# Optimization experiments

Measured on AMD Instinct MI355X. Metric: run time of the kernel, lower is better.

The kernel has to match this reference:

```python
import jax, jax.numpy as jnp
import numpy as np

HIDDEN = 1024
HEADS = 16
HEAD_DIM = HIDDEN // HEADS


def setup_inputs() -> dict:
    key = jax.random.key(0)
    kx, kq, kk, kv, ko = jax.random.split(key, 5)
    s = 1.0 / np.sqrt(HIDDEN)
    return {
        "x": jax.random.normal(kx, (2, 2048, HIDDEN), dtype=jnp.float32),
        "Wq": jax.random.normal(kq, (HIDDEN, HIDDEN), dtype=jnp.float32) * s,
        "Wk": jax.random.normal(kk, (HIDDEN, HIDDEN), dtype=jnp.float32) * s,
        "Wv": jax.random.normal(kv, (HIDDEN, HIDDEN), dtype=jnp.float32) * s,
        "Wo": jax.random.normal(ko, (HIDDEN, HIDDEN), dtype=jnp.float32) * s,
    }


def reference(x, Wq, Wk, Wv, Wo):
    B, T, C = x.shape
    H, D = HEADS, HEAD_DIM
    # projections (torch Linear: y = x @ W.T); weights here stored as (out,in)==(C,C)
    q = (x @ Wq.T).reshape(B, T, H, D)
    k = (x @ Wk.T).reshape(B, T, H, D)
    v = (x @ Wv.T).reshape(B, T, H, D)
    scale = 1.0 / np.sqrt(D).astype(np.float32)
    # scores: (B,H,T,T)
    attn = jnp.einsum("bqhd,bkhd->bhqk", q, k) * scale
    causal = jnp.tril(jnp.ones((T, T), dtype=bool))  # keep lower triangle
    attn = jnp.where(causal, attn, -jnp.inf)
    attn = jax.nn.softmax(attn, axis=-1)
    out = jnp.einsum("bhqk,bkhd->bqhd", attn, v).reshape(B, T, C)
    return out @ Wo.T
```

## Files before the change

### kernel.cpp

```cpp
#include <hip/hip_runtime.h>
#include <cstdint>
#include <cstddef>

#define HID 1024
#define NH 16
#define HD 64
#define SEQ 2048
#define BATCH 2

typedef __attribute__((ext_vector_type(8))) short bf16x8;
typedef __attribute__((ext_vector_type(4))) short bf16x4;
typedef bf16x8 __attribute__((may_alias)) bf16x8_ma;
typedef bf16x4 __attribute__((may_alias)) bf16x4_ma;
typedef uint4 __attribute__((may_alias)) uint4_ma;
typedef __attribute__((ext_vector_type(4))) float f32x4;

__device__ __forceinline__ unsigned short f2bf(float f){
  unsigned u = __builtin_bit_cast(unsigned, f);
  u += 0x7fffu + ((u >> 16) & 1u);
  return (unsigned short)(u >> 16);
}

__device__ __forceinline__ unsigned cvtpk_bf16(float lo, float hi){
  unsigned r;
  asm("v_cvt_pk_bf16_f32 %0, %1, %2" : "=v"(r) : "v"(lo), "v"(hi));
  return r;
}

__device__ __forceinline__ void gll(const unsigned short* g, unsigned short* l){
  __builtin_amdgcn_global_load_lds(
      (const __attribute__((address_space(1))) unsigned int*)(g),
      (__attribute__((address_space(3))) unsigned int*)(l),
      16, 0, 0);
}

__global__ __launch_bounds__(256) void cvt_all(
    const float* __restrict__ x,  const float* __restrict__ wq,
    const float* __restrict__ wk, const float* __restrict__ wv,
    const float* __restrict__ wo,
    unsigned short* __restrict__ xb,  unsigned short* __restrict__ wqb,
    unsigned short* __restrict__ wkb, unsigned short* __restrict__ wvb,
    unsigned short* __restrict__ wob)
{
  const size_t NX = (size_t)BATCH*SEQ*HID;
  const size_t NW = (size_t)HID*HID;
  size_t i = ((size_t)blockIdx.x*256 + threadIdx.x)*4;
  const float* src; unsigned short* dst; size_t off;
  if (i < NX) { src = x; dst = xb; off = i; }
  else {
    size_t j = i - NX; int w = (int)(j >> 20); off = j & (NW-1);
    if      (w==0){ src=wq; dst=wqb; }
    else if (w==1){ src=wk; dst=wkb; }
    else if (w==2){ src=wv; dst=wvb; }
    else          { src=wo; dst=wob; }
  }
  float4 v = *(const float4*)(src+off);
  uint2 p;
  p.x = (unsigned)f2bf(v.x) | ((unsigned)f2bf(v.y)<<16);
  p.y = (unsigned)f2bf(v.z) | ((unsigned)f2bf(v.w)<<16);
  *(uint2*)(dst+off) = p;
}

__global__ __launch_bounds__(256) void gemm_qkv(
    const unsigned short* __restrict__ A,
    const unsigned short* __restrict__ Bq,
    const unsigned short* __restrict__ Bk,
    const unsigned short* __restrict__ Bv,
    unsigned short* __restrict__ Qh,
    unsigned short* __restrict__ Kh,
    unsigned short* __restrict__ VhT)
{
  __shared__ unsigned short S[16384];
  const int tid = threadIdx.x;
  const int w = tid >> 6, lane = tid & 63, l15 = lane & 15, quad = lane >> 4;
  const int wm = (w >> 1)*64, wn = (w & 1)*64;
  const int bm = blockIdx.y*128;
  const int which = blockIdx.x >> 3;
  const int bn = (blockIdx.x & 7)*128;
  const unsigned short* B = which==0 ? Bq : (which==1 ? Bk : Bv);
  unsigned short* C       = which==0 ? Qh : (which==1 ? Kh : VhT);
  const float cscale      = which==0 ? 0.18033688011112042f : 1.0f;
  const int lrow = lane >> 2, lcol = (lane & 3)*8;

  f32x4 acc[4][4] = {};

  {
    #pragma unroll
    for (int p=0;p<2;p++){
      int c = w*2 + p;
      gll(&A[(size_t)(bm + c*16 + lrow)*HID + lcol], &S[c*512]);
      gll(&B[(size_t)(bn + c*16 + lrow)*HID + lcol], &S[8192 + c*512]);
    }
  }
  __syncthreads();

  int cur = 0;
  for (int kb=0; kb<32; ++kb){
    if (kb < 31){
      unsigned short* Ad = S + (cur^1)*4096;
      unsigned short* Bd = S + 8192 + (cur^1)*4096;
      #pragma unroll
      for (int p=0;p<2;p++){
        int c = w*2 + p;
        gll(&A[(size_t)(bm + c*16 + lrow)*HID + (kb+1)*32 + lcol], &Ad[c*512]);
        gll(&B[(size_t)(bn + c*16 + lrow)*HID + (kb+1)*32 + lcol], &Bd[c*512]);
      }
    }
    const unsigned short* Ac = S + cur*4096;
    const unsigned short* Bc = S + 8192 + cur*4096;
    bf16x8 af[4], bfr[4];
    #pragma unroll
    for (int i=0;i<4;i++) af[i]  = *(const bf16x8*)(&Ac[(wm + i*16 + l15)*32 + quad*8]);
    #pragma unroll
    for (int j=0;j<4;j++) bfr[j] = *(const bf16x8*)(&Bc[(wn + j*16 + l15)*32 + quad*8]);
    #pragma unroll
    for (int i=0;i<4;i++)
      #pragma unroll
      for (int j=0;j<4;j++)
        acc[i][j] = __builtin_amdgcn_mfma_f32_16x16x32_bf16(af[i], bfr[j], acc[i][j], 0,0,0);
    __syncthreads();
    cur ^= 1;
  }

  #pragma unroll
  for (int i=0;i<4;i++)
    #pragma unroll
    for (int j=0;j<4;j++)
      #pragma unroll
      for (int r=0;r<4;r++){
        int row = wm + i*16 + quad*4 + r;
        int col = wn + j*16 + l15;
        unsigned off = (unsigned)(row*256 + col*2);
        *(unsigned short*)((char*)S + (off ^ ((unsigned)(row & 7) << 4))) =
            f2bf(acc[i][j][r]*cscale);
      }
  __syncthreads();
  if (which < 2){
    #pragma unroll
    for (int pass=0; pass<8; ++pass){
      int tr    = pass*16 + (tid >> 4);
      int hf    = (tid >> 3) & 1;
      int blkin = tid & 7;
      unsigned off = (unsigned)(tr*256 + hf*128 + blkin*16);
      uint4 v = *(const uint4_ma*)((const char*)S + (off ^ ((unsigned)(tr & 7) << 4)));
      int m = bm + tr, b = m >> 11, t = m & (SEQ-1);
      int h = (bn >> 6) + hf;
      *(uint4*)(&C[(((size_t)(b*NH + h))*SEQ + t)*HD + blkin*8]) = v;
    }
  } else {
    const int b = bm >> 11, tb = bm & (SEQ-1);
    #pragma unroll
    for (int pass=0; pass<8; ++pass){
      int idx  = pass*256 + tid;
      int dcol = idx & 127;
      int tc   = idx >> 7;
      unsigned short tmp[8];
      #pragma unroll
      for (int j=0;j<8;j++){
        int r = tc*8 + j;
        unsigned off = (unsigned)(r*256 + dcol*2) ^ ((unsigned)j << 4);
        tmp[j] = *(const unsigned short*)((const char*)S + off);
      }
      int hh = (bn >> 6) + (dcol >> 6);
      int d  = dcol & 63;
      *(uint4*)(&C[(((size_t)(b*NH + hh))*HD + d)*SEQ + tb + tc*8]) = *(uint4_ma*)tmp;
    }
  }
}

__global__ __launch_bounds__(256) void gemm_out(
    const unsigned short* __restrict__ A,
    const unsigned short* __restrict__ B,
    float* __restrict__ C)
{
  __shared__ unsigned short As[8192];
  __shared__ unsigned short Bs[4096];
  const int tid = threadIdx.x;
  const int w = tid >> 6, lane = tid & 63, l15 = lane & 15, quad = lane >> 4;
  const int wm = (w >> 1)*64, wn = (w & 1)*32;
  const int bm = blockIdx.y*128, bn = blockIdx.x*64;
  const int lrow = lane >> 2, lcol = (lane & 3)*8;

  f32x4 acc[4][2] = {};
  for (int kb=0; kb<16; ++kb){
    __syncthreads();
    #pragma unroll
    for (int p=0;p<4;p++){
      int c = p*4 + w;
      int h = c >> 3, rb = c & 7;
      gll(&A[(size_t)(bm + rb*16 + lrow)*HID + kb*64 + h*32 + lcol], &As[h*4096 + rb*512]);
    }
    #pragma unroll
    for (int p=0;p<2;p++){
      int c = p*4 + w;
      int h = c >> 2, rb = c & 3;
      gll(&B[(size_t)(bn + rb*16 + lrow)*HID + kb*64 + h*32 + lcol], &Bs[h*2048 + rb*512]);
    }
    __syncthreads();
    #pragma unroll
    for (int kc=0;kc<2;kc++){
      bf16x8 af[4], bfr[2];
      #pragma unroll
      for (int i=0;i<4;i++) af[i]  = *(const bf16x8*)(&As[kc*4096 + (wm + i*16 + l15)*32 + quad*8]);
      #pragma unroll
      for (int j=0;j<2;j++) bfr[j] = *(const bf16x8*)(&Bs[kc*2048 + (wn + j*16 + l15)*32 + quad*8]);
      #pragma unroll
      for (int i=0;i<4;i++)
        #pragma unroll
        for (int j=0;j<2;j++)
          acc[i][j] = __builtin_amdgcn_mfma_f32_16x16x32_bf16(af[i], bfr[j], acc[i][j], 0,0,0);
    }
  }
  #pragma unroll
  for (int i=0;i<4;i++)
    #pragma unroll
    for (int j=0;j<2;j++)
      #pragma unroll
      for (int r=0;r<4;r++){
        int m = bm + wm + i*16 + quad*4 + r;
        int n = bn + wn + j*16 + l15;
        C[(size_t)m*HID + n] = acc[i][j][r];
      }
}

__global__ __launch_bounds__(256, 4) void attn(
    const unsigned short* __restrict__ Qh,
    const unsigned short* __restrict__ Kh,
    const unsigned short* __restrict__ VhT,
    unsigned short* __restrict__ Ao)
{
  __shared__ unsigned short QP[4096];
  __shared__ unsigned short Ks[2][4096];
  __shared__ unsigned short Vt[2][4096];

  const int bh = blockIdx.x;
  const int y  = blockIdx.y;
  const int tid = threadIdx.x;
  const int w = tid >> 6, lane = tid & 63, l15 = lane & 15, quad = lane >> 4;
  const int lrow = lane >> 2, lcol = (lane & 3)*8;

  const size_t base = (size_t)bh * SEQ * HD;
  const unsigned short* VTg = VhT + base;
  unsigned short* Psw = QP + w*1024;
  const unsigned swz = (unsigned)(l15 & 7) << 4;
  const int b = bh >> 4, h = bh & (NH-1);

  #pragma unroll 1
  for (int hf=0; hf<2; ++hf){
    const int qb = hf ? (31 - y) : y;
    const unsigned short* Qg = Qh + base + (size_t)qb*64*HD;

    __syncthreads();

    #pragma unroll
    for (int p=0;p<2;p++){
      int c = w*2 + p;
      gll(&Qg[(size_t)((c&3)*16 + lrow)*HD + (c>>2)*32 + lcol], &QP[(c>>2)*2048 + (c&3)*512]);
    }
    {
      const unsigned short* Kg = Kh + base;
      if (w < 2){
        #pragma unroll
        for (int p=0;p<4;p++){ int cc = w*4 + p;
          gll(&Kg[(size_t)((cc&3)*16 + lrow)*HD + (cc>>2)*32 + lcol], &Ks[0][(cc>>2)*2048 + (cc&3)*512]); }
      } else {
        #pragma unroll
        for (int p=0;p<4;p++){ int cc = (w-2)*4 + p;
          gll(&VTg[(size_t)((cc&3)*16 + lrow)*SEQ + (cc>>2)*32 + lcol], &Vt[0][(cc>>2)*2048 + (cc&3)*512]); }
      }
    }
    __syncthreads();
    bf16x8 qfrag[2];
    #pragma unroll
    for (int kc=0;kc<2;kc++)
      qfrag[kc] = *(const bf16x8*)(&QP[kc*2048 + (w*16 + l15)*32 + quad*8]);
    __syncthreads();

    f32x4 lacc = {0.f, 0.f, 0.f, 0.f};
    f32x4 oacc[4] = {};
    const int qrow = qb*64 + w*16 + l15;
    int cur = 0;

    for (int kb=0; kb<=qb; ++kb){
      if (kb < qb){
        const unsigned short* Kg2 = Kh + base + (size_t)(kb+1)*64*HD;
        unsigned short* Kd = Ks[cur^1];
        unsigned short* Vd = Vt[cur^1];
        if (w < 2){
          #pragma unroll
          for (int p=0;p<4;p++){ int cc = w*4 + p;
            gll(&Kg2[(size_t)((cc&3)*16 + lrow)*HD + (cc>>2)*32 + lcol], &Kd[(cc>>2)*2048 + (cc&3)*512]); }
        } else {
          #pragma unroll
          for (int p=0;p<4;p++){ int cc = (w-2)*4 + p;
            gll(&VTg[(size_t)((cc&3)*16 + lrow)*SEQ + (size_t)(kb+1)*64 + (cc>>2)*32 + lcol], &Vd[(cc>>2)*2048 + (cc&3)*512]); }
        }
      }

      const unsigned short* Ksc = Ks[cur];
      f32x4 s[4] = {};
      #pragma unroll
      for (int cb=0;cb<4;cb++)
        #pragma unroll
        for (int kc=0;kc<2;kc++){
          bf16x8 kfr = *(const bf16x8*)(&Ksc[kc*2048 + (cb*16 + l15)*32 + quad*8]);
          s[cb] = __builtin_amdgcn_mfma_f32_16x16x32_bf16(kfr, qfrag[kc], s[cb], 0,0,0);
        }

      if (kb == qb){
        #pragma unroll
        for (int cb=0;cb<4;cb++)
          #pragma unroll
          for (int r=0;r<4;r++){
            int t = kb*64 + cb*16 + quad*4 + r;
            if (t > qrow) s[cb][r] = -1e30f;
          }
      }
      #pragma unroll
      for (int cb=0;cb<4;cb++)
        #pragma unroll
        for (int r=0;r<4;r++)
          s[cb][r] = exp2f(s[cb][r]);
      lacc += (s[0] + s[1]) + (s[2] + s[3]);

      #pragma unroll
      for (int cb=0;cb<4;cb++){
        uint2 d2;
        d2.x = cvtpk_bf16(s[cb][0], s[cb][1]);
        d2.y = cvtpk_bf16(s[cb][2], s[cb][3]);
        *(bf16x4_ma*)((char*)Psw + (((unsigned)(l15*128 + cb*32 + quad*8)) ^ swz)) =
            __builtin_bit_cast(bf16x4, d2);
      }
      asm volatile("" ::: "memory");
      bf16x8 pa[2];
      #pragma unroll
      for (int kc=0;kc<2;kc++)
        pa[kc] = *(const bf16x8_ma*)((const char*)Psw + (((unsigned)(l15*128 + kc*64 + quad*16)) ^ swz));

      const unsigned short* Vtc = Vt[cur];
      #pragma unroll
      for (int db=0;db<4;db++)
        #pragma unroll
        for (int kc=0;kc<2;kc++){
          bf16x8 vfr = *(const bf16x8*)(&Vtc[kc*2048 + (db*16 + l15)*32 + quad*8]);
          oacc[db] = __builtin_amdgcn_mfma_f32_16x16x32_bf16(pa[kc], vfr, oacc[db], 0,0,0);
        }

      if (kb < qb) __syncthreads();
      cur ^= 1;
    }

    float l = (lacc[0] + lacc[1]) + (lacc[2] + lacc[3]);
    l += __shfl_xor(l, 16);
    l += __shfl_xor(l, 32);
    float inv[4];
    #pragma unroll
    for (int r=0;r<4;r++)
      inv[r] = 1.0f / __shfl(l, quad*4 + r);

    #pragma unroll
    for (int db=0;db<4;db++)
      #pragma unroll
      for (int r=0;r<4;r++){
        int t = qb*64 + w*16 + quad*4 + r;
        int col = h*HD + db*16 + l15;
        Ao[((size_t)b*SEQ + t)*HID + col] = f2bf(oacc[db][r] * inv[r]);
      }
  }
}

extern "C" void kernel_launch(void* const* d_in, const int* in_sizes, int n_in,
                              void* d_out, int out_size, void* d_ws, size_t ws_size,
                              hipStream_t stream)
{
  const float* x  = (const float*)d_in[0];
  const float* Wq = (const float*)d_in[1];
  const float* Wk = (const float*)d_in[2];
  const float* Wv = (const float*)d_in[3];
  const float* Wo = (const float*)d_in[4];

  unsigned short* xb  = (unsigned short*)d_ws;
  unsigned short* wqb = xb  + (size_t)4*1024*1024;
  unsigned short* wkb = wqb + (size_t)1024*1024;
  unsigned short* wvb = wkb + (size_t)1024*1024;
  unsigned short* wob = wvb + (size_t)1024*1024;
  unsigned short* Qh  = wob + (size_t)1024*1024;
  unsigned short* Kh  = Qh  + (size_t)4*1024*1024;
  unsigned short* Vh  = Kh  + (size_t)4*1024*1024;
  unsigned short* VhT = Vh  + (size_t)4*1024*1024;
  unsigned short* Ao  = xb;

  cvt_all<<<8192, 256, 0, stream>>>(x, Wq, Wk, Wv, Wo, xb, wqb, wkb, wvb, wob);

  gemm_qkv<<<dim3(24, 32), 256, 0, stream>>>(xb, wqb, wkb, wvb, Qh, Kh, VhT);

  attn<<<dim3(BATCH*NH, 16), 256, 0, stream>>>(Qh, Kh, VhT, Ao);

  gemm_out<<<dim3(16, 32), 256, 0, stream>>>(Ao, wob, (float*)d_out);
}
```

Baseline: 178.7 us.

## Triple-buffer K/V in attention, one query block per workgroup with balanced ordering

```diff
diff --git a/kernel.cpp b/kernel.cpp
--- a/kernel.cpp
+++ b/kernel.cpp
@@ -223,150 +223,156 @@
       }
 }
 
-__global__ __launch_bounds__(256, 4) void attn(
+__global__ __launch_bounds__(256, 2) void attn(
     const unsigned short* __restrict__ Qh,
     const unsigned short* __restrict__ Kh,
     const unsigned short* __restrict__ VhT,
     unsigned short* __restrict__ Ao)
 {
   __shared__ unsigned short QP[4096];
-  __shared__ unsigned short Ks[2][4096];
-  __shared__ unsigned short Vt[2][4096];
+  __shared__ unsigned short Ks[3][4096];
+  __shared__ unsigned short Vt[3][4096];
 
   const int bh = blockIdx.x;
   const int y  = blockIdx.y;
+  const int a = y & 7, bb = y >> 3;
+  const int qb = (bb & 1) ? (7 - a)*4 + bb : a*4 + bb;
   const int tid = threadIdx.x;
   const int w = tid >> 6, lane = tid & 63, l15 = lane & 15, quad = lane >> 4;
   const int lrow = lane >> 2, lcol = (lane & 3)*8;
 
   const size_t base = (size_t)bh * SEQ * HD;
+  const unsigned short* Qg  = Qh + base + (size_t)qb*64*HD;
+  const unsigned short* Kg  = Kh + base;
   const unsigned short* VTg = VhT + base;
   unsigned short* Psw = QP + w*1024;
   const unsigned swz = (unsigned)(l15 & 7) << 4;
-  const int b = bh >> 4, h = bh & (NH-1);
-
-  #pragma unroll 1
-  for (int hf=0; hf<2; ++hf){
-    const int qb = hf ? (31 - y) : y;
-    const unsigned short* Qg = Qh + base + (size_t)qb*64*HD;
-
-    __syncthreads();
-
-    #pragma unroll
-    for (int p=0;p<2;p++){
-      int c = w*2 + p;
-      gll(&Qg[(size_t)((c&3)*16 + lrow)*HD + (c>>2)*32 + lcol], &QP[(c>>2)*2048 + (c&3)*512]);
-    }
+
+  #pragma unroll
+  for (int p=0;p<2;p++){
+    int c = w*2 + p;
+    gll(&Qg[(size_t)((c&3)*16 + lrow)*HD + (c>>2)*32 + lcol], &QP[(c>>2)*2048 + (c&3)*512]);
+  }
+  {
+    const int t1 = qb > 0 ? 1 : 0;
+    if (w < 2){
+      #pragma unroll
+      for (int p=0;p<4;p++){ int cc = w*4 + p;
+        gll(&Kg[(size_t)((cc&3)*16 + lrow)*HD + (cc>>2)*32 + lcol], &Ks[0][(cc>>2)*2048 + (cc&3)*512]); }
+      #pragma unroll
+      for (int p=0;p<4;p++){ int cc = w*4 + p;
+        gll(&Kg[(size_t)(t1*64 + (cc&3)*16 + lrow)*HD + (cc>>2)*32 + lcol], &Ks[1][(cc>>2)*2048 + (cc&3)*512]); }
+    } else {
+      #pragma unroll
+      for (int p=0;p<4;p++){ int cc = (w-2)*4 + p;
+        gll(&VTg[(size_t)((cc&3)*16 + lrow)*SEQ + (cc>>2)*32 + lcol], &Vt[0][(cc>>2)*2048 + (cc&3)*512]); }
+      #pragma unroll
+      for (int p=0;p<4;p++){ int cc = (w-2)*4 + p;
+        gll(&VTg[(size_t)((cc&3)*16 + lrow)*SEQ + t1*64 + (cc>>2)*32 + lcol], &Vt[1][(cc>>2)*2048 + (cc&3)*512]); }
+    }
+  }
+  __syncthreads();
+  bf16x8 qfrag[2];
+  #pragma unroll
+  for (int kc=0;kc<2;kc++)
+    qfrag[kc] = *(const bf16x8*)(&QP[kc*2048 + (w*16 + l15)*32 + quad*8]);
+  __syncthreads();
+
+  f32x4 lacc = {0.f, 0.f, 0.f, 0.f};
+  f32x4 oacc[4] = {};
+  const int qrow = qb*64 + w*16 + l15;
+
+  unsigned short *K0 = Ks[0], *K1 = Ks[1], *K2 = Ks[2];
+  unsigned short *V0 = Vt[0], *V1 = Vt[1], *V2 = Vt[2];
+
+  for (int kb=0; kb<=qb; ++kb){
     {
-      const unsigned short* Kg = Kh + base;
+      const int tn = (kb+2 <= qb) ? (kb+2) : qb;
       if (w < 2){
         #pragma unroll
         for (int p=0;p<4;p++){ int cc = w*4 + p;
-          gll(&Kg[(size_t)((cc&3)*16 + lrow)*HD + (cc>>2)*32 + lcol], &Ks[0][(cc>>2)*2048 + (cc&3)*512]); }
+          gll(&Kg[(size_t)(tn*64 + (cc&3)*16 + lrow)*HD + (cc>>2)*32 + lcol], &K2[(cc>>2)*2048 + (cc&3)*512]); }
       } else {
         #pragma unroll
         for (int p=0;p<4;p++){ int cc = (w-2)*4 + p;
-          gll(&VTg[(size_t)((cc&3)*16 + lrow)*SEQ + (cc>>2)*32 + lcol], &Vt[0][(cc>>2)*2048 + (cc&3)*512]); }
-      }
-    }
-    __syncthreads();
-    bf16x8 qfrag[2];
-    #pragma unroll
-    for (int kc=0;kc<2;kc++)
-      qfrag[kc] = *(const bf16x8*)(&QP[kc*2048 + (w*16 + l15)*32 + quad*8]);
-    __syncthreads();
-
-    f32x4 lacc = {0.f, 0.f, 0.f, 0.f};
-    f32x4 oacc[4] = {};
-    const int qrow = qb*64 + w*16 + l15;
-    int cur = 0;
-
-    for (int kb=0; kb<=qb; ++kb){
-      if (kb < qb){
-        const unsigned short* Kg2 = Kh + base + (size_t)(kb+1)*64*HD;
-        unsigned short* Kd = Ks[cur^1];
-        unsigned short* Vd = Vt[cur^1];
-        if (w < 2){
-          #pragma unroll
-          for (int p=0;p<4;p++){ int cc = w*4 + p;
-            gll(&Kg2[(size_t)((cc&3)*16 + lrow)*HD + (cc>>2)*32 + lcol], &Kd[(cc>>2)*2048 + (cc&3)*512]); }
-        } else {
-          #pragma unroll
-          for (int p=0;p<4;p++){ int cc = (w-2)*4 + p;
-            gll(&VTg[(size_t)((cc&3)*16 + lrow)*SEQ + (size_t)(kb+1)*64 + (cc>>2)*32 + lcol], &Vd[(cc>>2)*2048 + (cc&3)*512]); }
-        }
-      }
-
-      const unsigned short* Ksc = Ks[cur];
-      f32x4 s[4] = {};
+          gll(&VTg[(size_t)((cc&3)*16 + lrow)*SEQ + (size_t)tn*64 + (cc>>2)*32 + lcol], &V2[(cc>>2)*2048 + (cc&3)*512]); }
+      }
+    }
+    __builtin_amdgcn_sched_barrier(0);
+
+    f32x4 s[4] = {};
+    #pragma unroll
+    for (int cb=0;cb<4;cb++)
+      #pragma unroll
+      for (int kc=0;kc<2;kc++){
+        bf16x8 kfr = *(const bf16x8*)(&K0[kc*2048 + (cb*16 + l15)*32 + quad*8]);
+        s[cb] = __builtin_amdgcn_mfma_f32_16x16x32_bf16(kfr, qfrag[kc], s[cb], 0,0,0);
+      }
+
+    if (kb == qb){
       #pragma unroll
       for (int cb=0;cb<4;cb++)
         #pragma unroll
-        for (int kc=0;kc<2;kc++){
-          bf16x8 kfr = *(const bf16x8*)(&Ksc[kc*2048 + (cb*16 + l15)*32 + quad*8]);
-          s[cb] = __builtin_amdgcn_mfma_f32_16x16x32_bf16(kfr, qfrag[kc], s[cb], 0,0,0);
+        for (int r=0;r<4;r++){
+          int t = kb*64 + cb*16 + quad*4 + r;
+          if (t > qrow) s[cb][r] = -1e30f;
         }
-
-      if (kb == qb){
-        #pragma unroll
-        for (int cb=0;cb<4;cb++)
-          #pragma unroll
-          for (int r=0;r<4;r++){
-            int t = kb*64 + cb*16 + quad*4 + r;
-            if (t > qrow) s[cb][r] = -1e30f;
-          }
-      }
-      #pragma unroll
-      for (int cb=0;cb<4;cb++)
-        #pragma unroll
-        for (int r=0;r<4;r++)
-          s[cb][r] = exp2f(s[cb][r]);
-      lacc += (s[0] + s[1]) + (s[2] + s[3]);
-
-      #pragma unroll
-      for (int cb=0;cb<4;cb++){
-        uint2 d2;
-        d2.x = cvtpk_bf16(s[cb][0], s[cb][1]);
-        d2.y = cvtpk_bf16(s[cb][2], s[cb][3]);
-        *(bf16x4_ma*)((char*)Psw + (((unsigned)(l15*128 + cb*32 + quad*8)) ^ swz)) =
-            __builtin_bit_cast(bf16x4, d2);
-      }
-      asm volatile("" ::: "memory");
-      bf16x8 pa[2];
-      #pragma unroll
-      for (int kc=0;kc<2;kc++)
-        pa[kc] = *(const bf16x8_ma*)((const char*)Psw + (((unsigned)(l15*128 + kc*64 + quad*16)) ^ swz));
-
-      const unsigned short* Vtc = Vt[cur];
-      #pragma unroll
-      for (int db=0;db<4;db++)
-        #pragma unroll
-        for (int kc=0;kc<2;kc++){
-          bf16x8 vfr = *(const bf16x8*)(&Vtc[kc*2048 + (db*16 + l15)*32 + quad*8]);
-          oacc[db] = __builtin_amdgcn_mfma_f32_16x16x32_bf16(pa[kc], vfr, oacc[db], 0,0,0);
-        }
-
-      if (kb < qb) __syncthreads();
-      cur ^= 1;
-    }
-
-    float l = (lacc[0] + lacc[1]) + (lacc[2] + lacc[3]);
-    l += __shfl_xor(l, 16);
-    l += __shfl_xor(l, 32);
-    float inv[4];
-    #pragma unroll
-    for (int r=0;r<4;r++)
-      inv[r] = 1.0f / __shfl(l, quad*4 + r);
+    }
+    #pragma unroll
+    for (int cb=0;cb<4;cb++)
+      #pragma unroll
+      for (int r=0;r<4;r++)
+        s[cb][r] = exp2f(s[cb][r]);
+    lacc += (s[0] + s[1]) + (s[2] + s[3]);
+
+    #pragma unroll
+    for (int cb=0;cb<4;cb++){
+      uint2 d2;
+      d2.x = cvtpk_bf16(s[cb][0], s[cb][1]);
+      d2.y = cvtpk_bf16(s[cb][2], s[cb][3]);
+      *(bf16x4_ma*)((char*)Psw + (((unsigned)(l15*128 + cb*32 + quad*8)) ^ swz)) =
+          __builtin_bit_cast(bf16x4, d2);
+    }
+    asm volatile("" ::: "memory");
+    bf16x8 pa[2];
+    #pragma unroll
+    for (int kc=0;kc<2;kc++)
+      pa[kc] = *(const bf16x8_ma*)((const char*)Psw + (((unsigned)(l15*128 + kc*64 + quad*16)) ^ swz));
 
     #pragma unroll
     for (int db=0;db<4;db++)
       #pragma unroll
-      for (int r=0;r<4;r++){
-        int t = qb*64 + w*16 + quad*4 + r;
-        int col = h*HD + db*16 + l15;
-        Ao[((size_t)b*SEQ + t)*HID + col] = f2bf(oacc[db][r] * inv[r]);
-      }
-  }
+      for (int kc=0;kc<2;kc++){
+        bf16x8 vfr = *(const bf16x8*)(&V0[kc*2048 + (db*16 + l15)*32 + quad*8]);
+        oacc[db] = __builtin_amdgcn_mfma_f32_16x16x32_bf16(pa[kc], vfr, oacc[db], 0,0,0);
+      }
+
+    asm volatile("s_waitcnt vmcnt(4)" ::: "memory");
+    __builtin_amdgcn_s_barrier();
+    __builtin_amdgcn_sched_barrier(0);
+
+    unsigned short* tk = K0; K0 = K1; K1 = K2; K2 = tk;
+    unsigned short* tv = V0; V0 = V1; V1 = V2; V2 = tv;
+  }
+  asm volatile("s_waitcnt vmcnt(0)" ::: "memory");
+
+  float l = (lacc[0] + lacc[1]) + (lacc[2] + lacc[3]);
+  l += __shfl_xor(l, 16);
+  l += __shfl_xor(l, 32);
+  float inv[4];
+  #pragma unroll
+  for (int r=0;r<4;r++)
+    inv[r] = 1.0f / __shfl(l, quad*4 + r);
+
+  const int b = bh >> 4, h = bh & (NH-1);
+  #pragma unroll
+  for (int db=0;db<4;db++)
+    #pragma unroll
+    for (int r=0;r<4;r++){
+      int t = qb*64 + w*16 + quad*4 + r;
+      int col = h*HD + db*16 + l15;
+      Ao[((size_t)b*SEQ + t)*HID + col] = f2bf(oacc[db][r] * inv[r]);
+    }
 }
 
 extern "C" void kernel_launch(void* const* d_in, const int* in_sizes, int n_in,
@@ -394,7 +400,7 @@
 
   gemm_qkv<<<dim3(24, 32), 256, 0, stream>>>(xb, wqb, wkb, wvb, Qh, Kh, VhT);
 
-  attn<<<dim3(BATCH*NH, 16), 256, 0, stream>>>(Qh, Kh, VhT, Ao);
+  attn<<<dim3(BATCH*NH, SEQ/64), 256, 0, stream>>>(Qh, Kh, VhT, Ao);
 
   gemm_out<<<dim3(16, 32), 256, 0, stream>>>(Ao, wob, (float*)d_out);
 }
```

New measurement: 185.7 us. 1.04x slower.

## Double-buffer output GEMM loads and split attention into one query block per workgroup

Applied to the files above, without the earlier changes.

```diff
diff --git a/kernel.cpp b/kernel.cpp
--- a/kernel.cpp
+++ b/kernel.cpp
@@ -173,8 +173,7 @@
     const unsigned short* __restrict__ B,
     float* __restrict__ C)
 {
-  __shared__ unsigned short As[8192];
-  __shared__ unsigned short Bs[4096];
+  __shared__ unsigned short S[12288];
   const int tid = threadIdx.x;
   const int w = tid >> 6, lane = tid & 63, l15 = lane & 15, quad = lane >> 4;
   const int wm = (w >> 1)*64, wn = (w & 1)*32;
@@ -182,35 +181,45 @@
   const int lrow = lane >> 2, lcol = (lane & 3)*8;
 
   f32x4 acc[4][2] = {};
-  for (int kb=0; kb<16; ++kb){
+
+  {
+    #pragma unroll
+    for (int p=0;p<2;p++){
+      int c = w*2 + p;
+      gll(&A[(size_t)(bm + c*16 + lrow)*HID + lcol], &S[c*512]);
+    }
+    gll(&B[(size_t)(bn + w*16 + lrow)*HID + lcol], &S[8192 + w*512]);
+  }
+  __syncthreads();
+
+  int cur = 0;
+  for (int kb=0; kb<32; ++kb){
+    if (kb < 31){
+      unsigned short* Ad = S + (cur^1)*4096;
+      unsigned short* Bd = S + 8192 + (cur^1)*2048;
+      #pragma unroll
+      for (int p=0;p<2;p++){
+        int c = w*2 + p;
+        gll(&A[(size_t)(bm + c*16 + lrow)*HID + (kb+1)*32 + lcol], &Ad[c*512]);
+      }
+      gll(&B[(size_t)(bn + w*16 + lrow)*HID + (kb+1)*32 + lcol], &Bd[w*512]);
+    }
+    const unsigned short* Ac = S + cur*4096;
+    const unsigned short* Bc = S + 8192 + cur*2048;
+    bf16x8 af[4], bfr[2];
+    #pragma unroll
+    for (int i=0;i<4;i++) af[i]  = *(const bf16x8*)(&Ac[(wm + i*16 + l15)*32 + quad*8]);
+    #pragma unroll
+    for (int j=0;j<2;j++) bfr[j] = *(const bf16x8*)(&Bc[(wn + j*16 + l15)*32 + quad*8]);
+    #pragma unroll
+    for (int i=0;i<4;i++)
+      #pragma unroll
+      for (int j=0;j<2;j++)
+        acc[i][j] = __builtin_amdgcn_mfma_f32_16x16x32_bf16(af[i], bfr[j], acc[i][j], 0,0,0);
     __syncthreads();
-    #pragma unroll
-    for (int p=0;p<4;p++){
-      int c = p*4 + w;
-      int h = c >> 3, rb = c & 7;
-      gll(&A[(size_t)(bm + rb*16 + lrow)*HID + kb*64 + h*32 + lcol], &As[h*4096 + rb*512]);
-    }
-    #pragma unroll
-    for (int p=0;p<2;p++){
-      int c = p*4 + w;
-      int h = c >> 2, rb = c & 3;
-      gll(&B[(size_t)(bn + rb*16 + lrow)*HID + kb*64 + h*32 + lcol], &Bs[h*2048 + rb*512]);
-    }
-    __syncthreads();
-    #pragma unroll
-    for (int kc=0;kc<2;kc++){
-      bf16x8 af[4], bfr[2];
-      #pragma unroll
-      for (int i=0;i<4;i++) af[i]  = *(const bf16x8*)(&As[kc*4096 + (wm + i*16 + l15)*32 + quad*8]);
-      #pragma unroll
-      for (int j=0;j<2;j++) bfr[j] = *(const bf16x8*)(&Bs[kc*2048 + (wn + j*16 + l15)*32 + quad*8]);
-      #pragma unroll
-      for (int i=0;i<4;i++)
-        #pragma unroll
-        for (int j=0;j<2;j++)
-          acc[i][j] = __builtin_amdgcn_mfma_f32_16x16x32_bf16(af[i], bfr[j], acc[i][j], 0,0,0);
-    }
-  }
+    cur ^= 1;
+  }
+
   #pragma unroll
   for (int i=0;i<4;i++)
     #pragma unroll
@@ -235,138 +244,133 @@
 
   const int bh = blockIdx.x;
   const int y  = blockIdx.y;
+  const int a = y & 7, bb = y >> 3;
+  const int qb = (bb & 1) ? (7 - a)*4 + bb : a*4 + bb;
   const int tid = threadIdx.x;
   const int w = tid >> 6, lane = tid & 63, l15 = lane & 15, quad = lane >> 4;
   const int lrow = lane >> 2, lcol = (lane & 3)*8;
 
   const size_t base = (size_t)bh * SEQ * HD;
+  const unsigned short* Qg  = Qh + base + (size_t)qb*64*HD;
   const unsigned short* VTg = VhT + base;
   unsigned short* Psw = QP + w*1024;
   const unsigned swz = (unsigned)(l15 & 7) << 4;
-  const int b = bh >> 4, h = bh & (NH-1);
-
-  #pragma unroll 1
-  for (int hf=0; hf<2; ++hf){
-    const int qb = hf ? (31 - y) : y;
-    const unsigned short* Qg = Qh + base + (size_t)qb*64*HD;
-
-    __syncthreads();
-
-    #pragma unroll
-    for (int p=0;p<2;p++){
-      int c = w*2 + p;
-      gll(&Qg[(size_t)((c&3)*16 + lrow)*HD + (c>>2)*32 + lcol], &QP[(c>>2)*2048 + (c&3)*512]);
-    }
-    {
-      const unsigned short* Kg = Kh + base;
+
+  #pragma unroll
+  for (int p=0;p<2;p++){
+    int c = w*2 + p;
+    gll(&Qg[(size_t)((c&3)*16 + lrow)*HD + (c>>2)*32 + lcol], &QP[(c>>2)*2048 + (c&3)*512]);
+  }
+  {
+    const unsigned short* Kg = Kh + base;
+    if (w < 2){
+      #pragma unroll
+      for (int p=0;p<4;p++){ int cc = w*4 + p;
+        gll(&Kg[(size_t)((cc&3)*16 + lrow)*HD + (cc>>2)*32 + lcol], &Ks[0][(cc>>2)*2048 + (cc&3)*512]); }
+    } else {
+      #pragma unroll
+      for (int p=0;p<4;p++){ int cc = (w-2)*4 + p;
+        gll(&VTg[(size_t)((cc&3)*16 + lrow)*SEQ + (cc>>2)*32 + lcol], &Vt[0][(cc>>2)*2048 + (cc&3)*512]); }
+    }
+  }
+  __syncthreads();
+  bf16x8 qfrag[2];
+  #pragma unroll
+  for (int kc=0;kc<2;kc++)
+    qfrag[kc] = *(const bf16x8*)(&QP[kc*2048 + (w*16 + l15)*32 + quad*8]);
+  __syncthreads();
+
+  f32x4 lacc = {0.f, 0.f, 0.f, 0.f};
+  f32x4 oacc[4] = {};
+  const int qrow = qb*64 + w*16 + l15;
+  int cur = 0;
+
+  for (int kb=0; kb<=qb; ++kb){
+    if (kb < qb){
+      const unsigned short* Kg2 = Kh + base + (size_t)(kb+1)*64*HD;
+      unsigned short* Kd = Ks[cur^1];
+      unsigned short* Vd = Vt[cur^1];
       if (w < 2){
         #pragma unroll
         for (int p=0;p<4;p++){ int cc = w*4 + p;
-          gll(&Kg[(size_t)((cc&3)*16 + lrow)*HD + (cc>>2)*32 + lcol], &Ks[0][(cc>>2)*2048 + (cc&3)*512]); }
+          gll(&Kg2[(size_t)((cc&3)*16 + lrow)*HD + (cc>>2)*32 + lcol], &Kd[(cc>>2)*2048 + (cc&3)*512]); }
       } else {
         #pragma unroll
         for (int p=0;p<4;p++){ int cc = (w-2)*4 + p;
-          gll(&VTg[(size_t)((cc&3)*16 + lrow)*SEQ + (cc>>2)*32 + lcol], &Vt[0][(cc>>2)*2048 + (cc&3)*512]); }
-      }
-    }
-    __syncthreads();
-    bf16x8 qfrag[2];
-    #pragma unroll
-    for (int kc=0;kc<2;kc++)
-      qfrag[kc] = *(const bf16x8*)(&QP[kc*2048 + (w*16 + l15)*32 + quad*8]);
-    __syncthreads();
-
-    f32x4 lacc = {0.f, 0.f, 0.f, 0.f};
-    f32x4 oacc[4] = {};
-    const int qrow = qb*64 + w*16 + l15;
-    int cur = 0;
-
-    for (int kb=0; kb<=qb; ++kb){
-      if (kb < qb){
-        const unsigned short* Kg2 = Kh + base + (size_t)(kb+1)*64*HD;
-        unsigned short* Kd = Ks[cur^1];
-        unsigned short* Vd = Vt[cur^1];
-        if (w < 2){
-          #pragma unroll
-          for (int p=0;p<4;p++){ int cc = w*4 + p;
-            gll(&Kg2[(size_t)((cc&3)*16 + lrow)*HD + (cc>>2)*32 + lcol], &Kd[(cc>>2)*2048 + (cc&3)*512]); }
-        } else {
-          #pragma unroll
-          for (int p=0;p<4;p++){ int cc = (w-2)*4 + p;
-            gll(&VTg[(size_t)((cc&3)*16 + lrow)*SEQ + (size_t)(kb+1)*64 + (cc>>2)*32 + lcol], &Vd[(cc>>2)*2048 + (cc&3)*512]); }
-        }
-      }
-
-      const unsigned short* Ksc = Ks[cur];
-      f32x4 s[4] = {};
+          gll(&VTg[(size_t)((cc&3)*16 + lrow)*SEQ + (size_t)(kb+1)*64 + (cc>>2)*32 + lcol], &Vd[(cc>>2)*2048 + (cc&3)*512]); }
+      }
+    }
+
+    const unsigned short* Ksc = Ks[cur];
+    f32x4 s[4] = {};
+    #pragma unroll
+    for (int cb=0;cb<4;cb++)
+      #pragma unroll
+      for (int kc=0;kc<2;kc++){
+        bf16x8 kfr = *(const bf16x8*)(&Ksc[kc*2048 + (cb*16 + l15)*32 + quad*8]);
+        s[cb] = __builtin_amdgcn_mfma_f32_16x16x32_bf16(kfr, qfrag[kc], s[cb], 0,0,0);
+      }
+
+    if (kb == qb){
       #pragma unroll
       for (int cb=0;cb<4;cb++)
         #pragma unroll
-        for (int kc=0;kc<2;kc++){
-          bf16x8 kfr = *(const bf16x8*)(&Ksc[kc*2048 + (cb*16 + l15)*32 + quad*8]);
-          s[cb] = __builtin_amdgcn_mfma_f32_16x16x32_bf16(kfr, qfrag[kc], s[cb], 0,0,0);
+        for (int r=0;r<4;r++){
+          int t = kb*64 + cb*16 + quad*4 + r;
+          if (t > qrow) s[cb][r] = -1e30f;
         }
-
-      if (kb == qb){
-        #pragma unroll
-        for (int cb=0;cb<4;cb++)
-          #pragma unroll
-          for (int r=0;r<4;r++){
-            int t = kb*64 + cb*16 + quad*4 + r;
-            if (t > qrow) s[cb][r] = -1e30f;
-          }
-      }
-      #pragma unroll
-      for (int cb=0;cb<4;cb++)
-        #pragma unroll
-        for (int r=0;r<4;r++)
-          s[cb][r] = exp2f(s[cb][r]);
-      lacc += (s[0] + s[1]) + (s[2] + s[3]);
-
-      #pragma unroll
-      for (int cb=0;cb<4;cb++){
-        uint2 d2;
-        d2.x = cvtpk_bf16(s[cb][0], s[cb][1]);
-        d2.y = cvtpk_bf16(s[cb][2], s[cb][3]);
-        *(bf16x4_ma*)((char*)Psw + (((unsigned)(l15*128 + cb*32 + quad*8)) ^ swz)) =
-            __builtin_bit_cast(bf16x4, d2);
-      }
-      asm volatile("" ::: "memory");
-      bf16x8 pa[2];
-      #pragma unroll
-      for (int kc=0;kc<2;kc++)
-        pa[kc] = *(const bf16x8_ma*)((const char*)Psw + (((unsigned)(l15*128 + kc*64 + quad*16)) ^ swz));
-
-      const unsigned short* Vtc = Vt[cur];
-      #pragma unroll
-      for (int db=0;db<4;db++)
-        #pragma unroll
-        for (int kc=0;kc<2;kc++){
-          bf16x8 vfr = *(const bf16x8*)(&Vtc[kc*2048 + (db*16 + l15)*32 + quad*8]);
-          oacc[db] = __builtin_amdgcn_mfma_f32_16x16x32_bf16(pa[kc], vfr, oacc[db], 0,0,0);
-        }
-
-      if (kb < qb) __syncthreads();
-      cur ^= 1;
-    }
-
-    float l = (lacc[0] + lacc[1]) + (lacc[2] + lacc[3]);
-    l += __shfl_xor(l, 16);
-    l += __shfl_xor(l, 32);
-    float inv[4];
-    #pragma unroll
-    for (int r=0;r<4;r++)
-      inv[r] = 1.0f / __shfl(l, quad*4 + r);
-
+    }
+    #pragma unroll
+    for (int cb=0;cb<4;cb++)
+      #pragma unroll
+      for (int r=0;r<4;r++)
+        s[cb][r] = exp2f(s[cb][r]);
+    lacc += (s[0] + s[1]) + (s[2] + s[3]);
+
+    #pragma unroll
+    for (int cb=0;cb<4;cb++){
+      uint2 d2;
+      d2.x = cvtpk_bf16(s[cb][0], s[cb][1]);
+      d2.y = cvtpk_bf16(s[cb][2], s[cb][3]);
+      *(bf16x4_ma*)((char*)Psw + (((unsigned)(l15*128 + cb*32 + quad*8)) ^ swz)) =
+          __builtin_bit_cast(bf16x4, d2);
+    }
+    asm volatile("" ::: "memory");
+    bf16x8 pa[2];
+    #pragma unroll
+    for (int kc=0;kc<2;kc++)
+      pa[kc] = *(const bf16x8_ma*)((const char*)Psw + (((unsigned)(l15*128 + kc*64 + quad*16)) ^ swz));
+
+    const unsigned short* Vtc = Vt[cur];
     #pragma unroll
     for (int db=0;db<4;db++)
       #pragma unroll
-      for (int r=0;r<4;r++){
-        int t = qb*64 + w*16 + quad*4 + r;
-        int col = h*HD + db*16 + l15;
-        Ao[((size_t)b*SEQ + t)*HID + col] = f2bf(oacc[db][r] * inv[r]);
-      }
-  }
+      for (int kc=0;kc<2;kc++){
+        bf16x8 vfr = *(const bf16x8*)(&Vtc[kc*2048 + (db*16 + l15)*32 + quad*8]);
+        oacc[db] = __builtin_amdgcn_mfma_f32_16x16x32_bf16(pa[kc], vfr, oacc[db], 0,0,0);
+      }
+
+    if (kb < qb) __syncthreads();
+    cur ^= 1;
+  }
+
+  float l = (lacc[0] + lacc[1]) + (lacc[2] + lacc[3]);
+  l += __shfl_xor(l, 16);
+  l += __shfl_xor(l, 32);
+  float inv[4];
+  #pragma unroll
+  for (int r=0;r<4;r++)
+    inv[r] = 1.0f / __shfl(l, quad*4 + r);
+
+  const int b = bh >> 4, h = bh & (NH-1);
+  #pragma unroll
+  for (int db=0;db<4;db++)
+    #pragma unroll
+    for (int r=0;r<4;r++){
+      int t = qb*64 + w*16 + quad*4 + r;
+      int col = h*HD + db*16 + l15;
+      Ao[((size_t)b*SEQ + t)*HID + col] = f2bf(oacc[db][r] * inv[r]);
+    }
 }
 
 extern "C" void kernel_launch(void* const* d_in, const int* in_sizes, int n_in,
@@ -394,7 +398,7 @@
 
   gemm_qkv<<<dim3(24, 32), 256, 0, stream>>>(xb, wqb, wkb, wvb, Qh, Kh, VhT);
 
-  attn<<<dim3(BATCH*NH, 16), 256, 0, stream>>>(Qh, Kh, VhT, Ao);
+  attn<<<dim3(BATCH*NH, SEQ/64), 256, 0, stream>>>(Qh, Kh, VhT, Ao);
 
   gemm_out<<<dim3(16, 32), 256, 0, stream>>>(Ao, wob, (float*)d_out);
 }
```

Result: no change. 176.8 us (-1.1%).
